# Kernel optimization log

Hardware: AMD Instinct MI355X
Metric: run time of the kernel (lower is better)

The kernel has to match this reference:

```python
import jax, jax.numpy as jnp
import numpy as np
import math

B, S, D, H = 16, 256, 1024, 16
DK = D // H
MAXLEN = 512


def _sinusoid_table(maxlen, dim):
    # rows for positions -maxlen .. maxlen-1  (2*maxlen rows)
    pos = jnp.arange(-maxlen, maxlen, dtype=jnp.float32)[:, None]
    i = jnp.arange(dim)
    angle = pos / jnp.power(10000.0, (2 * (i // 2)) / dim).astype(jnp.float32)
    return jnp.where(i % 2 == 0, jnp.sin(angle), jnp.cos(angle))


def setup_inputs() -> dict:
    key = jax.random.key(0)
    ks = jax.random.split(key, 13)
    std_qk = math.sqrt(2.0 / (D + DK))
    inp = {
        "x": jax.random.normal(ks[0], (B, S, D), jnp.float32),
        "Wq": jax.random.normal(ks[1], (D, D), jnp.float32) * std_qk,
        "bq": jnp.zeros((D,), jnp.float32),
        "Wk": jax.random.normal(ks[2], (D, D), jnp.float32) * std_qk,
        "bk": jnp.zeros((D,), jnp.float32),
        "Wv": jax.random.normal(ks[3], (D, D), jnp.float32) * std_qk,
        "bv": jnp.zeros((D,), jnp.float32),
        "Wr": jax.random.normal(ks[4], (D, D), jnp.float32) * std_qk,
        "br": jnp.zeros((D,), jnp.float32),
        "u_bias": jax.random.normal(ks[5], (H, DK), jnp.float32) * math.sqrt(2.0 / (H + DK)),
        "v_bias": jax.random.normal(ks[6], (H, DK), jnp.float32) * math.sqrt(2.0 / (H + DK)),
        "Wo": jax.random.normal(ks[7], (D, D), jnp.float32) * math.sqrt(2.0 / (D + D)),
        "bo": jnp.zeros((D,), jnp.float32),
    }
    return inp


def reference(x, Wq, bq, Wk, bk, Wv, bv, Wr, br, u_bias, v_bias, Wo, bo):
    table = _sinusoid_table(MAXLEN, D)  # (2*MAXLEN, D)
    # relative position indices: idx[s, z] = z - s, shifted by +MAXLEN
    relpos_idx = (jnp.arange(2 * S)[None, :] - jnp.arange(S)[:, None])[:, :S] + MAXLEN
    relpos_vec = table[relpos_idx]  # (S, S, D)

    q = (x @ Wq.T + bq).reshape(B, S, H, DK)
    k = (x @ Wk.T + bk).reshape(B, S, H, DK)
    v = (x @ Wv.T + bv).reshape(B, S, H, DK)

    rp_k = (relpos_vec @ Wk.T + bk).reshape(S, S, H, DK)       # shared k_proj
    kR = (x @ Wr.T + br).reshape(B, S, H, DK)                  # relpos_k_proj(keys)
    rp_R = (relpos_vec @ Wr.T + br).reshape(S, S, H, DK)       # relpos_k_proj(relpos)

    w = jnp.einsum('bshd,bzhd->bhsz', q, k)
    w = w + jnp.einsum('bshd,szhd->bhsz', q, rp_k)
    w = w + jnp.einsum('hd,bzhd->bhz', u_bias, kR)[:, :, None, :]
    w = w + jnp.einsum('hd,szhd->hsz', v_bias, rp_R)[None, :, :, :]
    w = w / math.sqrt(DK)

    causal = jnp.tril(jnp.ones((S, S), jnp.float32))[None, None, :, :]
    w = w + jnp.log(causal)  # -inf above diagonal

    attn = jax.nn.softmax(w, axis=-1)                          # (B,H,S,S)
    vw = jnp.einsum('bhsz,bzhd->bshd', attn, v).reshape(B, S, D)
    return vw @ Wo.T + bo
```

## Files before the change

### kernel.cpp

```cpp
#include <hip/hip_runtime.h>
#include <math.h>

constexpr int kB  = 16;
constexpr int kS  = 256;
constexpr int kD  = 1024;
constexpr int kH  = 16;
constexpr float kScale = 0.125f;

using bf16x8  = __attribute__((ext_vector_type(8))) short;
using floatx4 = __attribute__((ext_vector_type(4))) float;
typedef unsigned short u16;

__device__ __forceinline__ u16 f2bf(float x) {
  union { float f; unsigned u; } v; v.f = x;
  unsigned r = v.u + 0x7fffu + ((v.u >> 16) & 1u);
  return (u16)(r >> 16);
}
__device__ __forceinline__ float bf2f(u16 h) {
  union { unsigned u; float f; } v; v.u = ((unsigned)h) << 16;
  return v.f;
}

#define MFMA16(a, b, c) __builtin_amdgcn_mfma_f32_16x16x32_bf16((a), (b), (c), 0, 0, 0)
#define GLL16(gp, lp)                                                        \
  __builtin_amdgcn_global_load_lds(                                          \
      (const __attribute__((address_space(1))) unsigned int*)(gp),           \
      (__attribute__((address_space(3))) unsigned int*)(lp), 16, 0, 0)

__global__ __launch_bounds__(256) void pack_k(
    const float* __restrict__ x, const float* __restrict__ Wq,
    const float* __restrict__ Wk, const float* __restrict__ Wv,
    const float* __restrict__ Wo,
    const float* __restrict__ bq, const float* __restrict__ bk,
    const float* __restrict__ bv,
    u16* __restrict__ xA, u16* __restrict__ W3b, u16* __restrict__ Wob,
    float* __restrict__ b3) {
  size_t i = ((size_t)blockIdx.x * 256 + threadIdx.x) * 4;
  const size_t NX = (size_t)4194304, NW = (size_t)1048576;
  const size_t BEND = NX + 4 * NW + 3072;
  const float* src;
  u16* dst;
  size_t o;
  if (i < NX) {
    src = x; dst = xA; o = i;
  } else if (i < NX + 3 * NW) {
    size_t j = i - NX;
    int sel = (int)(j >> 20);
    o = j & (NW - 1);
    src = sel == 0 ? Wq : sel == 1 ? Wv : Wk;
    dst = W3b + (size_t)sel * NW;
  } else if (i < NX + 4 * NW) {
    o = i - NX - 3 * NW;
    src = Wo; dst = Wob;
  } else if (i < BEND) {
    size_t j = i - NX - 4 * NW;
    int sel = (int)(j >> 10);
    o = j & 1023;
    src = sel == 0 ? bq : sel == 1 ? bv : bk;
    *reinterpret_cast<float4*>(b3 + j) = *reinterpret_cast<const float4*>(src + o);
    return;
  } else if (i < BEND + 262144) {
    size_t j = i - BEND;
    int p = (int)(j >> 10);
    int ibase = (int)(j & 1023);
    ushort4 r;
    u16* rr = (u16*)&r;
#pragma unroll
    for (int c = 0; c < 4; ++c) {
      int idx = ibase + c;
      float ex = (float)(2 * (idx / 2)) * (1.0f / 1024.0f);
      float scale = exp2f(ex * -13.287712379549449f);
      float angle = (float)(p - 255) * scale;
      rr[c] = f2bf((idx & 1) ? cosf(angle) : sinf(angle));
    }
    *reinterpret_cast<ushort4*>(xA + NX + j) = r;
    return;
  } else {
    return;
  }
  float4 v = *reinterpret_cast<const float4*>(src + o);
  ushort4 r;
  r.x = f2bf(v.x); r.y = f2bf(v.y); r.z = f2bf(v.z); r.w = f2bf(v.w);
  *reinterpret_cast<ushort4*>(dst + o) = r;
}

__global__ __launch_bounds__(256) void uv_fold_k(
    const float* __restrict__ Wr, const float* __restrict__ br,
    const float* __restrict__ ub, const float* __restrict__ vb,
    u16* __restrict__ W3b, float* __restrict__ b3) {
  int gid = blockIdx.x * 256 + threadIdx.x;
  int j = gid >> 10, c = gid & 1023;
  int h = j & 15;
  const float* bvec = (j < 16 ? ub : vb) + h * 64;
  const float* wcol = Wr + (size_t)(h * 64) * 1024 + c;
  float a = 0.f;
#pragma unroll
  for (int d = 0; d < 64; ++d) a += bvec[d] * wcol[(size_t)d * 1024];
  W3b[(size_t)(3072 + j) * 1024 + c] = f2bf(a);
  if (gid < 128) {
    float s = 0.f;
    if (gid < 32) {
      const float* bv2 = (gid < 16 ? ub : vb) + (gid & 15) * 64;
      const float* brp = br + (gid & 15) * 64;
      for (int d = 0; d < 64; ++d) s += bv2[d] * brp[d];
    }
    b3[3072 + gid] = s;
  }
}

template <int OUT_MODE>
__global__ __launch_bounds__(256) void gemm_k(
    const u16* __restrict__ A, const u16* __restrict__ W,
    const float* __restrict__ bias, void* __restrict__ Cv,
    int M, int N, int K, float* __restrict__ utb, float* __restrict__ dtb,
    int mTiles, int nTiles) {
  const int xcd = blockIdx.x & 7;
  const int li  = blockIdx.x >> 3;
  const int r0   = (xcd * mTiles) >> 3;
  const int rcnt = (((xcd + 1) * mTiles) >> 3) - r0;
  if (li >= rcnt * nTiles) return;
  const int bm = (r0 + li % rcnt) * 128;
  const int bn = (li / rcnt) * 128;

  __shared__ u16 Alds[128 * 64];
  __shared__ u16 Blds[128 * 64];
  const int t = threadIdx.x, w = t >> 6, l = t & 63;
  const int l15 = l & 15, quad = l >> 4;
  const int wm = w >> 1, wn = w & 1;
  const int lrow8 = l >> 3;
  const int kslot = l & 7;

  floatx4 acc[4][4] = {};

  for (int k0 = 0; k0 < K; k0 += 64) {
#pragma unroll
    for (int sg = 0; sg < 4; ++sg) {
      int mrow = sg * 32 + w * 8 + lrow8;
      int gk = (kslot ^ (mrow & 7)) << 3;
      GLL16(A + (size_t)(bm + mrow) * K + k0 + gk, Alds + (sg * 32 + w * 8) * 64);
      GLL16(W + (size_t)(bn + mrow) * K + k0 + gk, Blds + (sg * 32 + w * 8) * 64);
    }
    __syncthreads();
#pragma unroll
    for (int c = 0; c < 2; ++c) {
      bf16x8 af[4], bf[4];
#pragma unroll
      for (int mi = 0; mi < 4; ++mi) {
        int am = wm * 64 + mi * 16 + l15;
        af[mi] = *(const bf16x8*)(Alds + am * 64 + (((c * 4 + quad) ^ (am & 7)) << 3));
      }
#pragma unroll
      for (int ni = 0; ni < 4; ++ni) {
        int an = wn * 64 + ni * 16 + l15;
        bf[ni] = *(const bf16x8*)(Blds + an * 64 + (((c * 4 + quad) ^ (an & 7)) << 3));
      }
#pragma unroll
      for (int mi = 0; mi < 4; ++mi)
#pragma unroll
        for (int ni = 0; ni < 4; ++ni)
          acc[mi][ni] = MFMA16(af[mi], bf[ni], acc[mi][ni]);
    }
    __syncthreads();
  }

#pragma unroll
  for (int ni = 0; ni < 4; ++ni) {
    int col = bn + wn * 64 + ni * 16 + l15;
    float bv = bias[col];
#pragma unroll
    for (int mi = 0; mi < 4; ++mi) {
      int mrow = bm + wm * 64 + mi * 16 + quad * 4;
#pragma unroll
      for (int r = 0; r < 4; ++r) {
        float v = acc[mi][ni][r] + bv;
        int row = mrow + r;
        if (OUT_MODE == 0) {
          ((float*)Cv)[(size_t)row * N + col] = v;
        }
      }
    }
  }
}

#define PHASE_MFMA(aa, bb, mh, nh, LG)                                         \
  do {                                                                         \
    __builtin_amdgcn_s_barrier();                                              \
    asm volatile("s_waitcnt lgkmcnt(" #LG ")" ::: "memory");                   \
    __builtin_amdgcn_sched_barrier(0);                                         \
    __builtin_amdgcn_s_setprio(1);                                             \
    _Pragma("unroll") for (int kc = 0; kc < 2; ++kc)                           \
        _Pragma("unroll") for (int i = 0; i < 4; ++i)                          \
            _Pragma("unroll") for (int j = 0; j < 2; ++j)                      \
                acc[(mh) * 4 + i][(nh) * 2 + j] = MFMA16(                      \
                    aa[kc][i], bb[kc][j], acc[(mh) * 4 + i][(nh) * 2 + j]);    \
    __builtin_amdgcn_s_setprio(0);                                             \
  } while (0)

__global__ __launch_bounds__(512, 2) void gemm256_k(
    const u16* __restrict__ A, const u16* __restrict__ W,
    const float* __restrict__ bias, u16* __restrict__ Cv,
    int K, float* __restrict__ utb, float* __restrict__ dtb,
    int mTiles, int nTiles) {
  const int nwg = mTiles * nTiles;
  const int qq = nwg >> 3, rr8 = nwg & 7;
  const int xcd = blockIdx.x & 7;
  const int wgid = (xcd < rr8 ? xcd * (qq + 1) : rr8 * (qq + 1) + (xcd - rr8) * qq)
                   + (blockIdx.x >> 3);
  const int bm = (wgid / nTiles) * 256;
  const int bn = (wgid % nTiles) * 256;

  __shared__ u16 lds[2 * 32768];

  const int t = threadIdx.x, w = t >> 6, l = t & 63;
  const int l15 = l & 15, quad = l >> 4;
  const int wm = w >> 2, wn = w & 3;

  const int NT = K >> 6;
  floatx4 acc[8][4] = {};

  auto stage = [&](int kt, int h) {
    const u16* srcm = (h < 2) ? A : W;
    const int baser = ((h < 2) ? bm : bn) + (h & 1) * 128;
    u16* dst = lds + (kt & 1) * 32768 + h * 8192 + w * 512;
    const int k0 = kt << 6;
#pragma unroll
    for (int j = 0; j < 2; ++j) {
      int sub = w * 8 + (l >> 3) + j * 64;
      int gk = ((l & 7) ^ (sub & 7)) << 3;
      GLL16(srcm + (size_t)(baser + sub) * K + k0 + gk, dst + j * 4096);
    }
  };

  bf16x8 a0[2][4], a1[2][4], b0[2][2], b1[2][2];

  auto readA = [&](bf16x8 (&aa)[2][4], const u16* LA, int hh) {
#pragma unroll
    for (int i = 0; i < 4; ++i) {
      int am = wm * 128 + hh * 64 + i * 16 + l15;
      const u16* p = LA + am * 64;
      aa[0][i] = *(const bf16x8*)(p + ((quad ^ (am & 7)) << 3));
      aa[1][i] = *(const bf16x8*)(p + (((4 + quad) ^ (am & 7)) << 3));
    }
  };
  auto readB = [&](bf16x8 (&bb)[2][2], const u16* LB, int hh) {
#pragma unroll
    for (int j = 0; j < 2; ++j) {
      int an = wn * 64 + hh * 32 + j * 16 + l15;
      const u16* p = LB + an * 64;
      bb[0][j] = *(const bf16x8*)(p + ((quad ^ (an & 7)) << 3));
      bb[1][j] = *(const bf16x8*)(p + (((4 + quad) ^ (an & 7)) << 3));
    }
  };

  stage(0, 2); stage(0, 3); stage(0, 0); stage(0, 1);
  stage(1, 2); stage(1, 3); stage(1, 0);
  asm volatile("s_waitcnt vmcnt(6)" ::: "memory");
  __builtin_amdgcn_s_barrier();
  readA(a0, lds, 0);
  readB(b0, lds + 16384, 0);

  for (int kt = 0; kt < NT; ++kt) {
    const u16* LA = lds + (kt & 1) * 32768;
    const u16* LB = LA + 16384;

    readB(b1, LB, 1);
    if (kt + 1 < NT) stage(kt + 1, 1);
    PHASE_MFMA(a0, b0, 0, 0, 4);
    __builtin_amdgcn_s_barrier();

    readA(a1, LA, 1);
    PHASE_MFMA(a0, b1, 0, 1, 8);
    __builtin_amdgcn_s_barrier();

    if (kt + 2 < NT) stage(kt + 2, 2);
    PHASE_MFMA(a1, b0, 1, 0, 0);
    __builtin_amdgcn_s_barrier();

    if (kt + 2 < NT) {
      stage(kt + 2, 3); stage(kt + 2, 0);
      asm volatile("s_waitcnt vmcnt(6)" ::: "memory");
    } else {
      asm volatile("s_waitcnt vmcnt(0)" ::: "memory");
    }
    __builtin_amdgcn_s_barrier();
    asm volatile("s_waitcnt lgkmcnt(0)" ::: "memory");
    __builtin_amdgcn_sched_barrier(0);
    if (kt + 1 < NT) {
      const u16* LAn = lds + ((kt + 1) & 1) * 32768;
      readA(a0, LAn, 0);
      readB(b0, LAn + 16384, 0);
    }
    __builtin_amdgcn_s_setprio(1);
#pragma unroll
    for (int kc = 0; kc < 2; ++kc)
#pragma unroll
      for (int i = 0; i < 4; ++i)
#pragma unroll
        for (int j = 0; j < 2; ++j)
          acc[4 + i][2 + j] = MFMA16(a1[kc][i], b1[kc][j], acc[4 + i][2 + j]);
    __builtin_amdgcn_s_setprio(0);
    __builtin_amdgcn_s_barrier();
  }

  float* fl = (float*)lds;
#pragma unroll 1
  for (int half = 0; half < 2; ++half) {
    __syncthreads();
    if (wm == half) {
#pragma unroll
      for (int ni = 0; ni < 4; ++ni) {
        float bv = bias[bn + wn * 64 + ni * 16 + l15];
#pragma unroll
        for (int mi = 0; mi < 8; ++mi) {
#pragma unroll
          for (int r = 0; r < 4; ++r) {
            int lr = mi * 16 + quad * 4 + r;
            int c  = wn * 64 + ni * 16 + l15;
            int key = ((r ^ quad) & 3) << 4;
            fl[lr * 256 + (c ^ key)] = acc[mi][ni][r] + bv;
          }
        }
      }
    }
    __syncthreads();
#pragma unroll 1
    for (int cc = 0; cc < 4; ++cc) {
      int col0 = bn + cc * 64;
#pragma unroll
      for (int rr = 0; rr < 4; ++rr) {
        int lr = w * 16 + rr * 4 + quad;
        int key = ((rr ^ quad) & 3) << 4;
        float4 v = *(const float4*)&fl[lr * 256 + ((cc * 64 + (l15 << 2)) ^ key)];
        int grow = bm + half * 128 + lr;
        if (col0 < 3072) {
          ushort4 hv;
          hv.x = f2bf(v.x); hv.y = f2bf(v.y); hv.z = f2bf(v.z); hv.w = f2bf(v.w);
          int matsel = col0 >> 10;
          int hh2 = (col0 >> 6) & 15;
          if (grow < 4096) {
            int bb = grow >> 8, ss = grow & 255;
            *(ushort4*)(Cv + (size_t)matsel * 4194304 +
                        ((size_t)(((bb << 4) + hh2) << 8) + ss) * 64 + (l15 << 2)) = hv;
          } else if (matsel == 2) {
            int pp = grow - 4096;
            *(ushort4*)(Cv + (size_t)3 * 4194304 +
                        ((size_t)((hh2 << 8) + pp)) * 64 + (l15 << 2)) = hv;
          }
        } else if (col0 < 3104) {
#pragma unroll
          for (int e = 0; e < 4; ++e) {
            int col = col0 + (l15 << 2) + e;
            float vv = e == 0 ? v.x : e == 1 ? v.y : e == 2 ? v.z : v.w;
            if (col < 3088) {
              if (grow < 4096)
                utb[((grow >> 8) * 16 + (col - 3072)) * 256 + (grow & 255)] = vv;
            } else if (col < 3104) {
              if (grow >= 4096)
                dtb[(col - 3088) * 256 + (grow - 4096)] = vv;
            }
          }
        }
      }
    }
  }
}

__global__ __launch_bounds__(512, 2) void attn_k(
    const u16* __restrict__ Qh, const u16* __restrict__ Kh,
    const u16* __restrict__ Vh, const u16* __restrict__ RPKh,
    const float* __restrict__ ut, const float* __restrict__ dt,
    u16* __restrict__ vw) {
  __shared__ u16 Klds[256 * 64];
  __shared__ u16 Vt[64][280];
  __shared__ float Sc[32][257];
  __shared__ float Sc2[32][257];
  __shared__ float Ut[256], Dt[256], Rinv[32];

  const int bh = blockIdx.x;
  const int h = bh & 15;
  const int b = bh >> 4;
  const size_t bh256 = (size_t)bh << 8;

  const int t = threadIdx.x, w = t >> 6, l = t & 63;
  const int l15 = l & 15, quad = l >> 4;

  {
    const int lrow8 = l >> 3, kslot = l & 7;
#pragma unroll
    for (int i = 0; i < 4; ++i) {
      int row = w * 32 + i * 8 + lrow8;
      int gk = (kslot ^ (row & 7)) << 3;
      GLL16(Kh + (bh256 + row) * 64 + gk, Klds + (w * 32 + i * 8) * 64);
    }
  }
  {
    int z = t & 255, dh = t >> 8;
    const u16* gp = Vh + (bh256 + z) * 64 + dh * 32;
    ushort4 vv[8];
#pragma unroll
    for (int i = 0; i < 8; ++i) vv[i] = *(const ushort4*)(gp + i * 4);
#pragma unroll
    for (int i = 0; i < 8; ++i) {
      Vt[dh * 32 + i * 4 + 0][z] = vv[i].x;
      Vt[dh * 32 + i * 4 + 1][z] = vv[i].y;
      Vt[dh * 32 + i * 4 + 2][z] = vv[i].z;
      Vt[dh * 32 + i * 4 + 3][z] = vv[i].w;
    }
  }
  if (t < 256) Ut[t] = ut[bh256 + t];
  else         Dt[t - 256] = dt[((size_t)h << 8) + (t - 256)];
  __syncthreads();

  for (int st = 0; st < 8; ++st) {
    const int s0 = st * 32;

    bf16x8 qa[2][2];
#pragma unroll
    for (int rt = 0; rt < 2; ++rt) {
      const u16* qp = Qh + (bh256 + s0 + rt * 16 + l15) * 64 + quad * 8;
      qa[rt][0] = *(const bf16x8*)qp;
      qa[rt][1] = *(const bf16x8*)(qp + 32);
    }

    {
      int cnt = 0;
#pragma unroll
      for (int rt = 0; rt < 2; ++rt) {
        const int rB = s0 + rt * 16;
        const int nzt = 2 * st + rt + 1;
        for (int zt = 0; zt < nzt; ++zt, ++cnt) {
          if ((cnt & 7) != w) continue;
          const int zr = (zt << 4) + l15;
          const u16* krow = Klds + zr * 64;
          bf16x8 kb0 = *(const bf16x8*)(krow + ((quad ^ (zr & 7)) << 3));
          bf16x8 kb1 = *(const bf16x8*)(krow + (((quad + 4) ^ (zr & 7)) << 3));
          floatx4 acc = {};
          acc = MFMA16(qa[rt][0], kb0, acc);
          acc = MFMA16(qa[rt][1], kb1, acc);
          float u = Ut[zr];
#pragma unroll
          for (int r = 0; r < 4; ++r)
            Sc[rt * 16 + quad * 4 + r][zr] = acc[r] + u;
        }
        for (int j = 0; j < nzt; ++j, ++cnt) {
          if ((cnt & 7) != w) continue;
          const int pr = 240 - rB + (j << 4) + l15;
          const u16* rp = RPKh + ((size_t)(h << 8) + pr) * 64 + quad * 8;
          bf16x8 rb0 = *(const bf16x8*)rp;
          bf16x8 rb1 = *(const bf16x8*)(rp + 32);
          floatx4 acc = {};
          acc = MFMA16(qa[rt][0], rb0, acc);
          acc = MFMA16(qa[rt][1], rb1, acc);
          float dv = Dt[pr];
#pragma unroll
          for (int r = 0; r < 4; ++r)
            Sc2[rt * 16 + quad * 4 + r][pr] = acc[r] + dv;
        }
      }
    }
    __syncthreads();

    {
      const int row = w * 4 + (l >> 4);
      const int c16 = l & 15;
      const int s = s0 + row;
      const int zfill = 32 * (st + 1);
      float m = -1e30f;
      for (int z = c16; z <= s; z += 16)
        m = fmaxf(m, Sc[row][z] + Sc2[row][z - s + 255]);
      m = fmaxf(m, __shfl_xor(m, 1));
      m = fmaxf(m, __shfl_xor(m, 2));
      m = fmaxf(m, __shfl_xor(m, 4));
      m = fmaxf(m, __shfl_xor(m, 8));
      m *= kScale;
      float sum = 0.f;
      for (int z = c16; z < zfill; z += 16) {
        float e = 0.f;
        if (z <= s) {
          e = __expf((Sc[row][z] + Sc2[row][z - s + 255]) * kScale - m);
          sum += e;
        }
        Sc[row][z] = e;
      }
      sum += __shfl_xor(sum, 1);
      sum += __shfl_xor(sum, 2);
      sum += __shfl_xor(sum, 4);
      sum += __shfl_xor(sum, 8);
      if (c16 == 0) Rinv[row] = 1.f / sum;
    }
    __syncthreads();

    {
      const int strip = w >> 2, nt = w & 3;
      const int sB = s0 + strip * 16;
      floatx4 oacc = {};
      for (int kc = 0; kc <= st; ++kc) {
        const float* prow = &Sc[strip * 16 + l15][kc * 32 + quad * 8];
        bf16x8 pa;
        pa[0] = (short)f2bf(prow[0]); pa[1] = (short)f2bf(prow[1]);
        pa[2] = (short)f2bf(prow[2]); pa[3] = (short)f2bf(prow[3]);
        pa[4] = (short)f2bf(prow[4]); pa[5] = (short)f2bf(prow[5]);
        pa[6] = (short)f2bf(prow[6]); pa[7] = (short)f2bf(prow[7]);
        const u16* vp = &Vt[nt * 16 + l15][kc * 32 + quad * 8];
        bf16x8 vbf = *(const bf16x8*)vp;
        oacc = MFMA16(pa, vbf, oacc);
      }
#pragma unroll
      for (int r = 0; r < 4; ++r) {
        float ivr = Rinv[strip * 16 + quad * 4 + r];
        int srow = sB + quad * 4 + r;
        vw[(size_t)(b * 256 + srow) * 1024 + h * 64 + nt * 16 + l15] =
            f2bf(oacc[r] * ivr);
      }
    }
    __syncthreads();
  }
}

extern "C" void kernel_launch(void* const* d_in, const int* in_sizes, int n_in,
                              void* d_out, int out_size, void* d_ws, size_t ws_size,
                              hipStream_t stream) {
  const float* x  = (const float*)d_in[0];
  const float* Wq = (const float*)d_in[1];
  const float* bq = (const float*)d_in[2];
  const float* Wk = (const float*)d_in[3];
  const float* bk = (const float*)d_in[4];
  const float* Wv = (const float*)d_in[5];
  const float* bv = (const float*)d_in[6];
  const float* Wr = (const float*)d_in[7];
  const float* br = (const float*)d_in[8];
  const float* ub = (const float*)d_in[9];
  const float* vb = (const float*)d_in[10];
  const float* Wo = (const float*)d_in[11];
  const float* bo = (const float*)d_in[12];
  float* out = (float*)d_out;

  char* base = (char*)d_ws;
  size_t off = 0;
  auto alloc = [&](size_t bytes) {
    void* p = base + off;
    off += (bytes + 255) & ~(size_t)255;
    return p;
  };

  const size_t MAT = (size_t)4194304;
  u16*   xA    = (u16*)alloc((size_t)4352 * 1024 * 2);
  u16*   W3b   = (u16*)alloc((size_t)3328 * 1024 * 2);
  u16*   Wob   = (u16*)alloc((size_t)1024 * 1024 * 2);
  float* b3    = (float*)alloc((size_t)3328 * 4);
  u16*   Ph    = (u16*)alloc((3 * MAT + 262144) * 2);
  float* utb   = (float*)alloc((size_t)65536 * 4);
  float* dtb   = (float*)alloc((size_t)4096 * 4);
  u16*   vwb   = (u16*)alloc((size_t)4096 * 1024 * 2);

  u16* Qh   = Ph;
  u16* Vh   = Ph + MAT;
  u16* Kh   = Ph + 2 * MAT;
  u16* RPKh = Ph + 3 * MAT;

  pack_k<<<dim3(8451), dim3(256), 0, stream>>>(x, Wq, Wk, Wv, Wo, bq, bk, bv,
                                               xA, W3b, Wob, b3);
  uv_fold_k<<<dim3(128), dim3(256), 0, stream>>>(Wr, br, ub, vb, W3b, b3);

  gemm256_k<<<dim3(221), dim3(512), 0, stream>>>(xA, W3b, b3, Ph,
                                                 1024, utb, dtb, 17, 13);

  attn_k<<<dim3(256), dim3(512), 0, stream>>>(Qh, Kh, Vh, RPKh, utb, dtb, vwb);

  gemm_k<0><<<dim3(256), dim3(256), 0, stream>>>(vwb, Wob, bo, out,
                                                 4096, 1024, 1024, nullptr, nullptr,
                                                 32, 8);
}
```

Measured before the change: 221.1 us.

## Defer PV matmul to next stripe, fold relpos scores into Sc, store bf16 P

Restructures the attention kernel loop. The P·V MFMA for a stripe is deferred into the next iteration so it overlaps with the next QK computation, which removes one barrier per stripe. The relative-position scores are accumulated directly into Sc with a diagonal-shifted index instead of a separate Sc2 buffer, and the R-projection loads are software-prefetched one step ahead. Softmax writes packed bf16 probabilities into a new Pl buffer, so the PV stage no longer converts from fp32. The risks are read-modify-write ordering on Sc between the two phases, which relies on a barrier, and correctness of the shifted-index mapping.

```diff
diff --git a/kernel.cpp b/kernel.cpp
--- a/kernel.cpp
+++ b/kernel.cpp
@@ -8,6 +8,7 @@
 constexpr float kScale = 0.125f;
 
 using bf16x8  = __attribute__((ext_vector_type(8))) short;
+using bf16x4  = __attribute__((ext_vector_type(4))) short;
 using floatx4 = __attribute__((ext_vector_type(4))) float;
 typedef unsigned short u16;
 
@@ -372,8 +373,8 @@
     u16* __restrict__ vw) {
   __shared__ u16 Klds[256 * 64];
   __shared__ u16 Vt[64][280];
-  __shared__ float Sc[32][257];
-  __shared__ float Sc2[32][257];
+  __shared__ __align__(16) float Sc[32][266];
+  __shared__ __align__(16) u16 Pl[32][268];
   __shared__ float Ut[256], Dt[256], Rinv[32];
 
   const int bh = blockIdx.x;
@@ -411,10 +412,33 @@
   else         Dt[t - 256] = dt[((size_t)h << 8) + (t - 256)];
   __syncthreads();
 
+  bf16x8 qa[2][2];
+  const int strip = w >> 2, nt = w & 3;
+
+  auto pv_tile = [&](int stp) {
+    floatx4 oacc = {};
+    for (int kc = 0; kc <= stp; ++kc) {
+      const u16* pp = &Pl[strip * 16 + l15][kc * 32 + quad * 8];
+      bf16x4 plo = *(const bf16x4*)pp;
+      bf16x4 phi = *(const bf16x4*)(pp + 4);
+      bf16x8 pa = __builtin_shufflevector(plo, phi, 0, 1, 2, 3, 4, 5, 6, 7);
+      bf16x8 vbf = *(const bf16x8*)&Vt[nt * 16 + l15][kc * 32 + quad * 8];
+      oacc = MFMA16(pa, vbf, oacc);
+    }
+#pragma unroll
+    for (int r = 0; r < 4; ++r) {
+      float ivr = Rinv[strip * 16 + quad * 4 + r];
+      int srow = stp * 32 + strip * 16 + quad * 4 + r;
+      vw[(size_t)(b * 256 + srow) * 1024 + h * 64 + nt * 16 + l15] =
+          f2bf(oacc[r] * ivr);
+    }
+  };
+
   for (int st = 0; st < 8; ++st) {
     const int s0 = st * 32;
-
-    bf16x8 qa[2][2];
+    const int n0 = 2 * st + 1;
+    const int tot = 4 * st + 3;
+
 #pragma unroll
     for (int rt = 0; rt < 2; ++rt) {
       const u16* qp = Qh + (bh256 + s0 + rt * 16 + l15) * 64 + quad * 8;
@@ -422,65 +446,86 @@
       qa[rt][1] = *(const bf16x8*)(qp + 32);
     }
 
+    if (st > 0) pv_tile(st - 1);
+    for (int i = w; i < tot; i += 8) {
+      int rt = (i >= n0) ? 1 : 0;
+      int zt = rt ? i - n0 : i;
+      const int zr = (zt << 4) + l15;
+      const u16* krow = Klds + zr * 64;
+      bf16x8 kb0 = *(const bf16x8*)(krow + ((quad ^ (zr & 7)) << 3));
+      bf16x8 kb1 = *(const bf16x8*)(krow + (((quad + 4) ^ (zr & 7)) << 3));
+      floatx4 acc = {};
+      acc = MFMA16(qa[rt][0], kb0, acc);
+      acc = MFMA16(qa[rt][1], kb1, acc);
+      float u = Ut[zr];
+#pragma unroll
+      for (int r = 0; r < 4; ++r)
+        Sc[rt * 16 + quad * 4 + r][zr] = acc[r] + u;
+    }
+    __syncthreads();
+
     {
-      int cnt = 0;
-#pragma unroll
-      for (int rt = 0; rt < 2; ++rt) {
-        const int rB = s0 + rt * 16;
-        const int nzt = 2 * st + rt + 1;
-        for (int zt = 0; zt < nzt; ++zt, ++cnt) {
-          if ((cnt & 7) != w) continue;
-          const int zr = (zt << 4) + l15;
-          const u16* krow = Klds + zr * 64;
-          bf16x8 kb0 = *(const bf16x8*)(krow + ((quad ^ (zr & 7)) << 3));
-          bf16x8 kb1 = *(const bf16x8*)(krow + (((quad + 4) ^ (zr & 7)) << 3));
+      int i = w;
+      if (i < tot) {
+        int rt = (i >= n0) ? 1 : 0, j = rt ? i - n0 : i;
+        int pr = 240 - (s0 + rt * 16) + (j << 4) + l15;
+        const u16* rp = RPKh + ((size_t)(h << 8) + pr) * 64 + quad * 8;
+        bf16x8 rb0 = *(const bf16x8*)rp;
+        bf16x8 rb1 = *(const bf16x8*)(rp + 32);
+        while (true) {
+          int rt_c = rt, j_c = j, pr_c = pr;
+          bf16x8 c0 = rb0, c1 = rb1;
+          i += 8;
+          if (i < tot) {
+            rt = (i >= n0) ? 1 : 0; j = rt ? i - n0 : i;
+            pr = 240 - (s0 + rt * 16) + (j << 4) + l15;
+            const u16* rp2 = RPKh + ((size_t)(h << 8) + pr) * 64 + quad * 8;
+            rb0 = *(const bf16x8*)rp2;
+            rb1 = *(const bf16x8*)(rp2 + 32);
+          }
           floatx4 acc = {};
-          acc = MFMA16(qa[rt][0], kb0, acc);
-          acc = MFMA16(qa[rt][1], kb1, acc);
-          float u = Ut[zr];
-#pragma unroll
-          for (int r = 0; r < 4; ++r)
-            Sc[rt * 16 + quad * 4 + r][zr] = acc[r] + u;
+          acc = MFMA16(qa[rt_c][0], c0, acc);
+          acc = MFMA16(qa[rt_c][1], c1, acc);
+          float dv = Dt[pr_c];
+#pragma unroll
+          for (int r = 0; r < 4; ++r) {
+            int z = (j_c << 4) + l15 + 4 * quad + r - 15;
+            if (z >= 0)
+              Sc[rt_c * 16 + 4 * quad + r][z] += acc[r] + dv;
+          }
+          if (i >= tot) break;
         }
-        for (int j = 0; j < nzt; ++j, ++cnt) {
-          if ((cnt & 7) != w) continue;
-          const int pr = 240 - rB + (j << 4) + l15;
-          const u16* rp = RPKh + ((size_t)(h << 8) + pr) * 64 + quad * 8;
-          bf16x8 rb0 = *(const bf16x8*)rp;
-          bf16x8 rb1 = *(const bf16x8*)(rp + 32);
-          floatx4 acc = {};
-          acc = MFMA16(qa[rt][0], rb0, acc);
-          acc = MFMA16(qa[rt][1], rb1, acc);
-          float dv = Dt[pr];
-#pragma unroll
-          for (int r = 0; r < 4; ++r)
-            Sc2[rt * 16 + quad * 4 + r][pr] = acc[r] + dv;
-        }
       }
     }
     __syncthreads();
 
     {
-      const int row = w * 4 + (l >> 4);
+      const int g = l >> 4;
+      const int row = w + 8 * g;
       const int c16 = l & 15;
       const int s = s0 + row;
       const int zfill = 32 * (st + 1);
       float m = -1e30f;
-      for (int z = c16; z <= s; z += 16)
-        m = fmaxf(m, Sc[row][z] + Sc2[row][z - s + 255]);
+      for (int z0 = 2 * c16; z0 <= s; z0 += 32) {
+        float v0 = Sc[row][z0];
+        float v1 = Sc[row][z0 + 1];
+        m = fmaxf(m, v0);
+        if (z0 + 1 <= s) m = fmaxf(m, v1);
+      }
       m = fmaxf(m, __shfl_xor(m, 1));
       m = fmaxf(m, __shfl_xor(m, 2));
       m = fmaxf(m, __shfl_xor(m, 4));
       m = fmaxf(m, __shfl_xor(m, 8));
       m *= kScale;
       float sum = 0.f;
-      for (int z = c16; z < zfill; z += 16) {
-        float e = 0.f;
-        if (z <= s) {
-          e = __expf((Sc[row][z] + Sc2[row][z - s + 255]) * kScale - m);
-          sum += e;
-        }
-        Sc[row][z] = e;
+      for (int z0 = 2 * c16; z0 < zfill; z0 += 32) {
+        float v0 = Sc[row][z0];
+        float v1 = Sc[row][z0 + 1];
+        float e0 = (z0 <= s) ? __expf(v0 * kScale - m) : 0.f;
+        float e1 = (z0 + 1 <= s) ? __expf(v1 * kScale - m) : 0.f;
+        sum += e0 + e1;
+        unsigned pk = (unsigned)f2bf(e0) | ((unsigned)f2bf(e1) << 16);
+        *(unsigned*)&Pl[row][z0] = pk;
       }
       sum += __shfl_xor(sum, 1);
       sum += __shfl_xor(sum, 2);
@@ -489,32 +534,9 @@
       if (c16 == 0) Rinv[row] = 1.f / sum;
     }
     __syncthreads();
-
-    {
-      const int strip = w >> 2, nt = w & 3;
-      const int sB = s0 + strip * 16;
-      floatx4 oacc = {};
-      for (int kc = 0; kc <= st; ++kc) {
-        const float* prow = &Sc[strip * 16 + l15][kc * 32 + quad * 8];
-        bf16x8 pa;
-        pa[0] = (short)f2bf(prow[0]); pa[1] = (short)f2bf(prow[1]);
-        pa[2] = (short)f2bf(prow[2]); pa[3] = (short)f2bf(prow[3]);
-        pa[4] = (short)f2bf(prow[4]); pa[5] = (short)f2bf(prow[5]);
-        pa[6] = (short)f2bf(prow[6]); pa[7] = (short)f2bf(prow[7]);
-        const u16* vp = &Vt[nt * 16 + l15][kc * 32 + quad * 8];
-        bf16x8 vbf = *(const bf16x8*)vp;
-        oacc = MFMA16(pa, vbf, oacc);
-      }
-#pragma unroll
-      for (int r = 0; r < 4; ++r) {
-        float ivr = Rinv[strip * 16 + quad * 4 + r];
-        int srow = sB + quad * 4 + r;
-        vw[(size_t)(b * 256 + srow) * 1024 + h * 64 + nt * 16 + l15] =
-            f2bf(oacc[r] * ivr);
-      }
-    }
-    __syncthreads();
-  }
+  }
+
+  pv_tile(7);
 }
 
 extern "C" void kernel_launch(void* const* d_in, const int* in_sizes, int n_in,
```

Result: slower. 333.0 us (+50.6%).

## Emit transposed V from projection GEMM and restructure attention to per-wave row strips

Applied to the files above, without the earlier changes.

The projection GEMM epilogue now writes V already transposed (per batch-head, d-major over positions), so the attention kernel no longer stages K and V into LDS or transposes V. The attention kernel is rewritten so each wave owns two 16-row query strips, paired as w and 15-w to balance the causal work. Each wave reads K, relative-position keys and V^T straight from global memory into registers with double buffering, and keeps softmax and the PV MFMA inside the wave using a private LDS score buffer. This removes most block-wide barriers and the shared staging. The trade-off is more global or L2 traffic per wave and a less coalesced transposed store in the GEMM epilogue.

```diff
diff --git a/kernel.cpp b/kernel.cpp
--- a/kernel.cpp
+++ b/kernel.cpp
@@ -303,6 +303,7 @@
   }
 
   float* fl = (float*)lds;
+  u16* VTp = Cv + (size_t)4194304;
 #pragma unroll 1
   for (int half = 0; half < 2; ++half) {
     __syncthreads();
@@ -323,40 +324,64 @@
       }
     }
     __syncthreads();
+    if (bn >= 1024 && bn < 2048) {
+      if (bm < 4096) {
+        int bb = bm >> 8;
 #pragma unroll 1
-    for (int cc = 0; cc < 4; ++cc) {
-      int col0 = bn + cc * 64;
-#pragma unroll
-      for (int rr = 0; rr < 4; ++rr) {
-        int lr = w * 16 + rr * 4 + quad;
-        int key = ((rr ^ quad) & 3) << 4;
-        float4 v = *(const float4*)&fl[lr * 256 + ((cc * 64 + (l15 << 2)) ^ key)];
-        int grow = bm + half * 128 + lr;
-        if (col0 < 3072) {
-          ushort4 hv;
-          hv.x = f2bf(v.x); hv.y = f2bf(v.y); hv.z = f2bf(v.z); hv.w = f2bf(v.w);
-          int matsel = col0 >> 10;
-          int hh2 = (col0 >> 6) & 15;
-          if (grow < 4096) {
-            int bb = grow >> 8, ss = grow & 255;
-            *(ushort4*)(Cv + (size_t)matsel * 4194304 +
-                        ((size_t)(((bb << 4) + hh2) << 8) + ss) * 64 + (l15 << 2)) = hv;
-          } else if (matsel == 2) {
-            int pp = grow - 4096;
-            *(ushort4*)(Cv + (size_t)3 * 4194304 +
-                        ((size_t)((hh2 << 8) + pp)) * 64 + (l15 << 2)) = hv;
+        for (int p = 0; p < 8; ++p) {
+          int dl = p * 32 + (t >> 4);
+          int zl = (t & 15) * 8;
+          int col = bn + dl;
+          int hh2 = (col >> 6) & 15, dd = col & 63;
+          u16 hv[8];
+#pragma unroll
+          for (int e = 0; e < 8; ++e) {
+            int lr = zl + e;
+            int key = ((lr & 3) ^ ((lr >> 2) & 3)) << 4;
+            hv[e] = f2bf(fl[lr * 256 + (dl ^ key)]);
           }
-        } else if (col0 < 3104) {
-#pragma unroll
-          for (int e = 0; e < 4; ++e) {
-            int col = col0 + (l15 << 2) + e;
-            float vv = e == 0 ? v.x : e == 1 ? v.y : e == 2 ? v.z : v.w;
-            if (col < 3088) {
-              if (grow < 4096)
-                utb[((grow >> 8) * 16 + (col - 3072)) * 256 + (grow & 255)] = vv;
-            } else if (col < 3104) {
-              if (grow >= 4096)
-                dtb[(col - 3088) * 256 + (grow - 4096)] = vv;
+          u16* vp = VTp + ((size_t)((bb << 4) + hh2) * 64 + dd) * 256 +
+                    half * 128 + zl;
+          *(ushort4*)vp = *(ushort4*)&hv[0];
+          *(ushort4*)(vp + 4) = *(ushort4*)&hv[4];
+        }
+      }
+    } else {
+#pragma unroll 1
+      for (int cc = 0; cc < 4; ++cc) {
+        int col0 = bn + cc * 64;
+#pragma unroll
+        for (int rr = 0; rr < 4; ++rr) {
+          int lr = w * 16 + rr * 4 + quad;
+          int key = ((rr ^ quad) & 3) << 4;
+          float4 v = *(const float4*)&fl[lr * 256 + ((cc * 64 + (l15 << 2)) ^ key)];
+          int grow = bm + half * 128 + lr;
+          if (col0 < 3072) {
+            ushort4 hvv;
+            hvv.x = f2bf(v.x); hvv.y = f2bf(v.y); hvv.z = f2bf(v.z); hvv.w = f2bf(v.w);
+            int matsel = col0 >> 10;
+            int hh2 = (col0 >> 6) & 15;
+            if (grow < 4096) {
+              int bb = grow >> 8, ss = grow & 255;
+              *(ushort4*)(Cv + (size_t)matsel * 4194304 +
+                          ((size_t)(((bb << 4) + hh2) << 8) + ss) * 64 + (l15 << 2)) = hvv;
+            } else if (matsel == 2) {
+              int pp = grow - 4096;
+              *(ushort4*)(Cv + (size_t)3 * 4194304 +
+                          ((size_t)((hh2 << 8) + pp)) * 64 + (l15 << 2)) = hvv;
+            }
+          } else if (col0 < 3104) {
+#pragma unroll
+            for (int e = 0; e < 4; ++e) {
+              int col = col0 + (l15 << 2) + e;
+              float vv = e == 0 ? v.x : e == 1 ? v.y : e == 2 ? v.z : v.w;
+              if (col < 3088) {
+                if (grow < 4096)
+                  utb[((grow >> 8) * 16 + (col - 3072)) * 256 + (grow & 255)] = vv;
+              } else if (col < 3104) {
+                if (grow >= 4096)
+                  dtb[(col - 3088) * 256 + (grow - 4096)] = vv;
+              }
             }
           }
         }
@@ -367,14 +392,11 @@
 
 __global__ __launch_bounds__(512, 2) void attn_k(
     const u16* __restrict__ Qh, const u16* __restrict__ Kh,
-    const u16* __restrict__ Vh, const u16* __restrict__ RPKh,
+    const u16* __restrict__ VT, const u16* __restrict__ RPKh,
     const float* __restrict__ ut, const float* __restrict__ dt,
     u16* __restrict__ vw) {
-  __shared__ u16 Klds[256 * 64];
-  __shared__ u16 Vt[64][280];
-  __shared__ float Sc[32][257];
-  __shared__ float Sc2[32][257];
-  __shared__ float Ut[256], Dt[256], Rinv[32];
+  __shared__ float ScW[8][16 * 260];
+  __shared__ float Ut[256], Dt[256];
 
   const int bh = blockIdx.x;
   const int h = bh & 15;
@@ -384,136 +406,148 @@
   const int t = threadIdx.x, w = t >> 6, l = t & 63;
   const int l15 = l & 15, quad = l >> 4;
 
-  {
-    const int lrow8 = l >> 3, kslot = l & 7;
-#pragma unroll
-    for (int i = 0; i < 4; ++i) {
-      int row = w * 32 + i * 8 + lrow8;
-      int gk = (kslot ^ (row & 7)) << 3;
-      GLL16(Kh + (bh256 + row) * 64 + gk, Klds + (w * 32 + i * 8) * 64);
-    }
-  }
-  {
-    int z = t & 255, dh = t >> 8;
-    const u16* gp = Vh + (bh256 + z) * 64 + dh * 32;
-    ushort4 vv[8];
-#pragma unroll
-    for (int i = 0; i < 8; ++i) vv[i] = *(const ushort4*)(gp + i * 4);
-#pragma unroll
-    for (int i = 0; i < 8; ++i) {
-      Vt[dh * 32 + i * 4 + 0][z] = vv[i].x;
-      Vt[dh * 32 + i * 4 + 1][z] = vv[i].y;
-      Vt[dh * 32 + i * 4 + 2][z] = vv[i].z;
-      Vt[dh * 32 + i * 4 + 3][z] = vv[i].w;
-    }
-  }
   if (t < 256) Ut[t] = ut[bh256 + t];
   else         Dt[t - 256] = dt[((size_t)h << 8) + (t - 256)];
   __syncthreads();
 
-  for (int st = 0; st < 8; ++st) {
-    const int s0 = st * 32;
-
-    bf16x8 qa[2][2];
-#pragma unroll
-    for (int rt = 0; rt < 2; ++rt) {
-      const u16* qp = Qh + (bh256 + s0 + rt * 16 + l15) * 64 + quad * 8;
-      qa[rt][0] = *(const bf16x8*)qp;
-      qa[rt][1] = *(const bf16x8*)(qp + 32);
-    }
-
+  float* scw = &ScW[w][0];
+
+#pragma unroll 1
+  for (int sidx = 0; sidx < 2; ++sidx) {
+    const int s = sidx ? (15 - w) : w;
+    const int rB = s << 4;
+
+    bf16x8 qa0, qa1;
     {
-      int cnt = 0;
-#pragma unroll
-      for (int rt = 0; rt < 2; ++rt) {
-        const int rB = s0 + rt * 16;
-        const int nzt = 2 * st + rt + 1;
-        for (int zt = 0; zt < nzt; ++zt, ++cnt) {
-          if ((cnt & 7) != w) continue;
-          const int zr = (zt << 4) + l15;
-          const u16* krow = Klds + zr * 64;
-          bf16x8 kb0 = *(const bf16x8*)(krow + ((quad ^ (zr & 7)) << 3));
-          bf16x8 kb1 = *(const bf16x8*)(krow + (((quad + 4) ^ (zr & 7)) << 3));
-          floatx4 acc = {};
-          acc = MFMA16(qa[rt][0], kb0, acc);
-          acc = MFMA16(qa[rt][1], kb1, acc);
-          float u = Ut[zr];
-#pragma unroll
-          for (int r = 0; r < 4; ++r)
-            Sc[rt * 16 + quad * 4 + r][zr] = acc[r] + u;
+      const u16* qp = Qh + (bh256 + rB + l15) * 64 + quad * 8;
+      qa0 = *(const bf16x8*)qp;
+      qa1 = *(const bf16x8*)(qp + 32);
+    }
+    bf16x8 kA0, kA1, kB0, kB1, rA0, rA1, rB0, rB1;
+    {
+      const u16* kp = Kh + (bh256 + l15) * 64 + quad * 8;
+      kA0 = *(const bf16x8*)kp;
+      kA1 = *(const bf16x8*)(kp + 32);
+      const u16* rp = RPKh + (((size_t)h << 8) + 240 - rB + l15) * 64 + quad * 8;
+      rA0 = *(const bf16x8*)rp;
+      rA1 = *(const bf16x8*)(rp + 32);
+    }
+
+#pragma unroll
+    for (int j = 0; j < 16; ++j) {
+      if (j > s) break;
+      if (j + 1 <= s) {
+        const u16* kp = Kh + (bh256 + ((j + 1) << 4) + l15) * 64 + quad * 8;
+        const u16* rp = RPKh + (((size_t)h << 8) + 240 - rB + ((j + 1) << 4) + l15) * 64 + quad * 8;
+        if ((j + 1) & 1) {
+          kB0 = *(const bf16x8*)kp; kB1 = *(const bf16x8*)(kp + 32);
+          rB0 = *(const bf16x8*)rp; rB1 = *(const bf16x8*)(rp + 32);
+        } else {
+          kA0 = *(const bf16x8*)kp; kA1 = *(const bf16x8*)(kp + 32);
+          rA0 = *(const bf16x8*)rp; rA1 = *(const bf16x8*)(rp + 32);
         }
-        for (int j = 0; j < nzt; ++j, ++cnt) {
-          if ((cnt & 7) != w) continue;
-          const int pr = 240 - rB + (j << 4) + l15;
-          const u16* rp = RPKh + ((size_t)(h << 8) + pr) * 64 + quad * 8;
-          bf16x8 rb0 = *(const bf16x8*)rp;
-          bf16x8 rb1 = *(const bf16x8*)(rp + 32);
-          floatx4 acc = {};
-          acc = MFMA16(qa[rt][0], rb0, acc);
-          acc = MFMA16(qa[rt][1], rb1, acc);
-          float dv = Dt[pr];
-#pragma unroll
-          for (int r = 0; r < 4; ++r)
-            Sc2[rt * 16 + quad * 4 + r][pr] = acc[r] + dv;
+      }
+      bf16x8 k0 = (j & 1) ? kB0 : kA0;
+      bf16x8 k1 = (j & 1) ? kB1 : kA1;
+      bf16x8 r0 = (j & 1) ? rB0 : rA0;
+      bf16x8 r1 = (j & 1) ? rB1 : rA1;
+      {
+        floatx4 acc = {};
+        acc = MFMA16(qa0, k0, acc);
+        acc = MFMA16(qa1, k1, acc);
+        float u = Ut[(j << 4) + l15];
+#pragma unroll
+        for (int r = 0; r < 4; ++r)
+          scw[(4 * quad + r) * 260 + (j << 4) + l15] = acc[r] + u;
+      }
+      {
+        floatx4 acc = {};
+        acc = MFMA16(qa0, r0, acc);
+        acc = MFMA16(qa1, r1, acc);
+        float dv = Dt[240 - rB + (j << 4) + l15];
+#pragma unroll
+        for (int r = 0; r < 4; ++r) {
+          int z = (j << 4) + l15 + 4 * quad + r - 15;
+          if (z >= 0)
+            scw[(4 * quad + r) * 260 + z] += acc[r] + dv;
         }
       }
     }
-    __syncthreads();
-
+
+    const int kcmax = s >> 1;
+    const int Rabs = rB + l15;
+    float m = -1e30f;
+#pragma unroll
+    for (int kc = 0; kc < 8; ++kc) {
+      if (kc > kcmax) break;
+      const float* sp = scw + l15 * 260 + kc * 32 + quad * 8;
+      floatx4 v0 = *(const floatx4*)sp;
+      floatx4 v1 = *(const floatx4*)(sp + 4);
+#pragma unroll
+      for (int e = 0; e < 4; ++e) {
+        int z = kc * 32 + quad * 8 + e;
+        if (z <= Rabs) m = fmaxf(m, v0[e]);
+        if (z + 4 <= Rabs) m = fmaxf(m, v1[e]);
+      }
+    }
+    m = fmaxf(m, __shfl_xor(m, 16));
+    m = fmaxf(m, __shfl_xor(m, 32));
+    m *= kScale;
+
+    floatx4 oacc[4] = {};
+    float sum = 0.f;
+    bf16x8 vA[4], vB[4];
     {
-      const int row = w * 4 + (l >> 4);
-      const int c16 = l & 15;
-      const int s = s0 + row;
-      const int zfill = 32 * (st + 1);
-      float m = -1e30f;
-      for (int z = c16; z <= s; z += 16)
-        m = fmaxf(m, Sc[row][z] + Sc2[row][z - s + 255]);
-      m = fmaxf(m, __shfl_xor(m, 1));
-      m = fmaxf(m, __shfl_xor(m, 2));
-      m = fmaxf(m, __shfl_xor(m, 4));
-      m = fmaxf(m, __shfl_xor(m, 8));
-      m *= kScale;
-      float sum = 0.f;
-      for (int z = c16; z < zfill; z += 16) {
-        float e = 0.f;
-        if (z <= s) {
-          e = __expf((Sc[row][z] + Sc2[row][z - s + 255]) * kScale - m);
-          sum += e;
+      const u16* vp = VT + ((size_t)bh * 64 + l15) * 256 + quad * 8;
+#pragma unroll
+      for (int nt = 0; nt < 4; ++nt)
+        vA[nt] = *(const bf16x8*)(vp + (size_t)nt * 16 * 256);
+    }
+#pragma unroll
+    for (int kc = 0; kc < 8; ++kc) {
+      if (kc > kcmax) break;
+      if (kc + 1 <= kcmax) {
+        const u16* vp = VT + ((size_t)bh * 64 + l15) * 256 + (kc + 1) * 32 + quad * 8;
+        if ((kc + 1) & 1) {
+#pragma unroll
+          for (int nt = 0; nt < 4; ++nt)
+            vB[nt] = *(const bf16x8*)(vp + (size_t)nt * 16 * 256);
+        } else {
+#pragma unroll
+          for (int nt = 0; nt < 4; ++nt)
+            vA[nt] = *(const bf16x8*)(vp + (size_t)nt * 16 * 256);
         }
-        Sc[row][z] = e;
-      }
-      sum += __shfl_xor(sum, 1);
-      sum += __shfl_xor(sum, 2);
-      sum += __shfl_xor(sum, 4);
-      sum += __shfl_xor(sum, 8);
-      if (c16 == 0) Rinv[row] = 1.f / sum;
-    }
-    __syncthreads();
-
-    {
-      const int strip = w >> 2, nt = w & 3;
-      const int sB = s0 + strip * 16;
-      floatx4 oacc = {};
-      for (int kc = 0; kc <= st; ++kc) {
-        const float* prow = &Sc[strip * 16 + l15][kc * 32 + quad * 8];
-        bf16x8 pa;
-        pa[0] = (short)f2bf(prow[0]); pa[1] = (short)f2bf(prow[1]);
-        pa[2] = (short)f2bf(prow[2]); pa[3] = (short)f2bf(prow[3]);
-        pa[4] = (short)f2bf(prow[4]); pa[5] = (short)f2bf(prow[5]);
-        pa[6] = (short)f2bf(prow[6]); pa[7] = (short)f2bf(prow[7]);
-        const u16* vp = &Vt[nt * 16 + l15][kc * 32 + quad * 8];
-        bf16x8 vbf = *(const bf16x8*)vp;
-        oacc = MFMA16(pa, vbf, oacc);
-      }
-#pragma unroll
-      for (int r = 0; r < 4; ++r) {
-        float ivr = Rinv[strip * 16 + quad * 4 + r];
-        int srow = sB + quad * 4 + r;
-        vw[(size_t)(b * 256 + srow) * 1024 + h * 64 + nt * 16 + l15] =
-            f2bf(oacc[r] * ivr);
-      }
-    }
-    __syncthreads();
+      }
+      const float* sp = scw + l15 * 260 + kc * 32 + quad * 8;
+      floatx4 v0 = *(const floatx4*)sp;
+      floatx4 v1 = *(const floatx4*)(sp + 4);
+      bf16x8 pa;
+#pragma unroll
+      for (int e = 0; e < 4; ++e) {
+        int z = kc * 32 + quad * 8 + e;
+        float p0 = (z <= Rabs) ? __expf(v0[e] * kScale - m) : 0.f;
+        float p1 = (z + 4 <= Rabs) ? __expf(v1[e] * kScale - m) : 0.f;
+        sum += p0 + p1;
+        pa[e] = (short)f2bf(p0);
+        pa[e + 4] = (short)f2bf(p1);
+      }
+#pragma unroll
+      for (int nt = 0; nt < 4; ++nt)
+        oacc[nt] = MFMA16(pa, (kc & 1) ? vB[nt] : vA[nt], oacc[nt]);
+    }
+    sum += __shfl_xor(sum, 16);
+    sum += __shfl_xor(sum, 32);
+    float rinv = 1.f / sum;
+
+#pragma unroll
+    for (int r = 0; r < 4; ++r) {
+      float rs = __shfl(rinv, 4 * quad + r);
+      int row = rB + 4 * quad + r;
+#pragma unroll
+      for (int nt = 0; nt < 4; ++nt)
+        vw[(size_t)(b * 256 + row) * 1024 + h * 64 + nt * 16 + l15] =
+            f2bf(oacc[nt][r] * rs);
+    }
   }
 }
 
@@ -554,7 +588,7 @@
   u16*   vwb   = (u16*)alloc((size_t)4096 * 1024 * 2);
 
   u16* Qh   = Ph;
-  u16* Vh   = Ph + MAT;
+  u16* VTb  = Ph + MAT;
   u16* Kh   = Ph + 2 * MAT;
   u16* RPKh = Ph + 3 * MAT;
 
@@ -565,7 +599,7 @@
   gemm256_k<<<dim3(221), dim3(512), 0, stream>>>(xA, W3b, b3, Ph,
                                                  1024, utb, dtb, 17, 13);
 
-  attn_k<<<dim3(256), dim3(512), 0, stream>>>(Qh, Kh, Vh, RPKh, utb, dtb, vwb);
+  attn_k<<<dim3(256), dim3(512), 0, stream>>>(Qh, Kh, VTb, RPKh, utb, dtb, vwb);
 
   gemm_k<0><<<dim3(256), dim3(256), 0, stream>>>(vwb, Wob, bo, out,
                                                  4096, 1024, 1024, nullptr, nullptr,
```

Measured after the change: 209.6 us. -5.2%, faster.
